# Optimization experiments

Hardware: AMD Instinct MI355X
Metric: run time of the kernel (lower is better)

## Reference

```python
import jax, jax.numpy as jnp
import numpy as np

K = 3
STRIDE = 1
PAD = 1


def conv2d(x, w, b):
    # standard NCHW conv, stride 1, pad 1
    out = jax.lax.conv_general_dilated(
        x, w, (STRIDE, STRIDE), [(PAD, PAD), (PAD, PAD)],
        dimension_numbers=("NCHW", "OIHW", "NCHW"))
    return out + b[None, :, None, None]


def deform_conv2d(x, offset, mask, weight):
    # torchvision.ops.deform_conv2d semantics (offset_groups=1):
    # offset: [B, 2*K*K, Ho, Wo] laid out as (k, (y, x)) per kernel tap k (row-major)
    # mask:   [B, K*K, Ho, Wo]
    B, C, H, W = x.shape
    KK = K * K
    Ho, Wo = offset.shape[2:]
    off = offset.reshape(B, KK, 2, Ho, Wo)

    # base sampling positions: p = out*stride - pad + kernel_tap + offset
    tap_y = jnp.repeat(jnp.arange(K, dtype=x.dtype), K)  # [KK]
    tap_x = jnp.tile(jnp.arange(K, dtype=x.dtype), K)    # [KK]
    grid_y = jnp.arange(Ho, dtype=x.dtype) * STRIDE - PAD
    grid_x = jnp.arange(Wo, dtype=x.dtype) * STRIDE - PAD
    py = grid_y[None, None, :, None] + tap_y[None, :, None, None] + off[:, :, 0]  # [B,KK,Ho,Wo]
    px = grid_x[None, None, None, :] + tap_x[None, :, None, None] + off[:, :, 1]

    y0 = jnp.floor(py)
    x0 = jnp.floor(px)
    wy1 = py - y0  # fractional parts
    wx1 = px - x0

    xf = x.reshape(B, C, H * W)

    def gather(yi, xi):
        # zero-padding semantics: out-of-bounds corners contribute 0
        valid = (yi >= 0) & (yi <= H - 1) & (xi >= 0) & (xi <= W - 1)
        idx = (jnp.clip(yi, 0, H - 1) * W + jnp.clip(xi, 0, W - 1)).astype(jnp.int32)
        v = jnp.take_along_axis(xf, idx.reshape(B, 1, KK * Ho * Wo), axis=2)
        v = v.reshape(B, C, KK, Ho, Wo)
        return v * valid[:, None].astype(x.dtype)

    e = lambda a: a[:, None]  # [B,KK,Ho,Wo] -> [B,1,KK,Ho,Wo]
    sampled = (gather(y0, x0) * e((1 - wy1) * (1 - wx1))
               + gather(y0, x0 + 1) * e((1 - wy1) * wx1)
               + gather(y0 + 1, x0) * e(wy1 * (1 - wx1))
               + gather(y0 + 1, x0 + 1) * e(wy1 * wx1))
    sampled = sampled * mask[:, None]  # modulated, [B,C,KK,Ho,Wo]

    Cout = weight.shape[0]
    out = jnp.einsum("bckhw,ock->bohw", sampled, weight.reshape(Cout, C, KK))
    return out


def setup_inputs() -> dict:
    key = jax.random.key(0)
    ks = jax.random.split(key, 5)
    B, Cin, Cout, H, W = 4, 128, 256, 64, 64
    x = jax.random.normal(ks[0], (B, Cin, H, W), jnp.float32)
    # offset/modulator convs are zero-init in the module; use small random weights
    # so the deformable sampling path is actually exercised
    offset_w = jax.random.normal(ks[1], (2 * K * K, Cin, K, K), jnp.float32) * 0.02
    offset_b = jax.random.normal(ks[2], (2 * K * K,), jnp.float32) * 0.1
    mod_w = jax.random.normal(ks[3], (K * K, Cin, K, K), jnp.float32) * 0.02
    mod_b = jnp.zeros((K * K,), jnp.float32)
    weight = jax.random.normal(ks[4], (Cout, Cin, K, K), jnp.float32) * (1.0 / np.sqrt(Cin * K * K))
    return {"x": x, "offset_w": offset_w, "offset_b": offset_b,
            "mod_w": mod_w, "mod_b": mod_b, "weight": weight}


def reference(x, offset_w, offset_b, mod_w, mod_b, weight):
    H, W = x.shape[2], x.shape[3]
    max_offset = max(H, W) / 4.0
    offset = jnp.clip(conv2d(x, offset_w, offset_b), -max_offset, max_offset)
    mask = 2.0 * jax.nn.sigmoid(conv2d(x, mod_w, mod_b))
    return deform_conv2d(x, offset, mask, weight)
```

## Files before the change

### kernel.cpp

```cpp
#include <hip/hip_runtime.h>
#include <math.h>

#define CIN   128
#define COUT  256
#define HH    64
#define WW    64
#define BB    4
#define KK    9
#define CK    (CIN*KK)

typedef unsigned short u16;
typedef unsigned int   u32;
using f32x4  = __attribute__((ext_vector_type(4))) float;
using s16x8  = __attribute__((ext_vector_type(8))) short;

__device__ __forceinline__ u16 f2bf(float f) {
    union { float f; u32 u; } v; v.f = f;
    u32 u = v.u;
    u += 0x7FFFu + ((u >> 16) & 1u);
    return (u16)(u >> 16);
}
__device__ __forceinline__ float bfel(s16x8 v, int j) {
    union { u32 u; float f; } c; c.u = ((u32)(u16)v[j]) << 16; return c.f;
}
__device__ __forceinline__ u32 asu(float f) {
    union { float f; u32 u; } v; v.f = f; return v.u;
}

__global__ __launch_bounds__(256)
void prep_all(const float* __restrict__ x, const float* __restrict__ w,
              const float* __restrict__ ow, const float* __restrict__ mw,
              u16* __restrict__ xt, u16* __restrict__ wfrag,
              u16* __restrict__ wofsf) {
    __shared__ u16 T[64][130];
    int blk = blockIdx.x;
    int tid = threadIdx.x;

    if (blk < 256) {
        int b = blk >> 6, y = blk & 63;
        int lane = tid & 63, cw = tid >> 6;
        for (int c = cw; c < 128; c += 4)
            T[lane][c] = f2bf(x[((b * 128 + c) * 64 + y) * 64 + lane]);
        __syncthreads();
        int c = tid & 127;
        for (int p = tid >> 7; p < 64; p += 2)
            xt[((b * 64 + y) * 64 + p) * 128 + c] = T[p][c];
    } else if (blk < 256 + 1152) {
        int i = (blk - 256) * 256 + tid;
        int j    = i & 7;
        int lane = (i >> 3) & 63;
        int ks4  = (i >> 9) & 3;
        int t    = (i >> 11) & 1;
        int wv   = (i >> 12) & 7;
        int tap  = i >> 15;
        int co = (wv * 2 + t) * 16 + (lane & 15);
        int k  = tap * 128 + ks4 * 32 + (lane >> 4) * 8 + j;
        int c  = k & 127;
        wfrag[i] = f2bf(w[co * CK + c * 9 + tap]);
    } else {
        int i = (blk - 1408) * 256 + tid;
        if (i < 9 * 4096) {
            int j    = i & 7;
            int lane = (i >> 3) & 63;
            int ks4  = (i >> 9) & 3;
            int t    = (i >> 11) & 1;
            int tap  = i >> 12;
            int co = t * 16 + (lane & 15);
            int k  = tap * 128 + ks4 * 32 + (lane >> 4) * 8 + j;
            int c  = k & 127;
            float v = 0.f;
            if (co < 18)      v = ow[co * CK + c * 9 + tap];
            else if (co < 27) v = mw[(co - 18) * CK + c * 9 + tap];
            wofsf[i] = f2bf(v);
        }
    }
}

__global__ __launch_bounds__(512, 4)
void dcn_fused(const u16* __restrict__ xt, const u16* __restrict__ wofsf,
               const float* __restrict__ ob, const float* __restrict__ mb,
               const u16* __restrict__ wfrag, float* __restrict__ out) {
    int blkid = blockIdx.x;
    int xcd = blkid & 7, idx = blkid >> 3;
    int b   = xcd >> 1;
    int ho  = ((xcd & 1) << 5) + (idx >> 1);
    int wo0 = (idx & 1) << 5;
    int tid = threadIdx.x;

    __shared__ __align__(16) u16 Sm[2][32][136];
    __shared__ float s_om[27][32];
    __shared__ int   s_idx[32][KK][4];
    __shared__ float s_wgt[32][KK][4];

    int wv   = tid >> 6, lane = tid & 63;
    int quad = lane >> 4, l16 = lane & 15;
    int gpx  = wv * 4 + (lane >> 4);
    int oct  = lane & 15;

    const u16* xtb = xt + (size_t)b * 4096 * 128;
    const s16x8 vzero = {0,0,0,0,0,0,0,0};

    int pa_ph = wv & 1;
    f32x4 aco[2];
    aco[0] = (f32x4)(0.f); aco[1] = (f32x4)(0.f);

    s16x8 sreg[2];
    auto pa_gather = [&](int tap, int slot) {
        int kx = tap % 3;
        int y  = ho - 1 + tap / 3;
        bool yok = (unsigned)y < HH;
        int col = wo0 + gpx + kx - 1;
        bool ok = yok && ((unsigned)col < WW);
        int yc = yok ? y : 0;
        int cc = ((unsigned)col < WW) ? col : 0;
        s16x8 v = *(const s16x8*)(xtb + (size_t)(yc * 64 + cc) * 128 + oct * 8);
        sreg[slot] = ok ? v : vzero;
    };

    pa_gather(0, 0);
    pa_gather(1, 1);
    int buf = 0;
#pragma unroll
    for (int tap = 0; tap < 9; ++tap) {
        int sl = tap & 1;
        *(s16x8*)(&Sm[buf][gpx][oct * 8]) = sreg[sl];
        __syncthreads();
        if (tap + 2 < 9) pa_gather(tap + 2, sl);

        if (wv < 2) {
            const u16* wc = wofsf + tap * 4096 + lane * 8;
#pragma unroll
            for (int ks4 = 0; ks4 < 4; ++ks4) {
                s16x8 bfrag = *(const s16x8*)(&Sm[buf][pa_ph * 16 + l16][ks4 * 32 + quad * 8]);
#pragma unroll
                for (int t = 0; t < 2; ++t) {
                    s16x8 afrag = *(const s16x8*)(wc + (t * 4 + ks4) * 512);
                    aco[t] = __builtin_amdgcn_mfma_f32_16x16x32_bf16(afrag, bfrag, aco[t], 0, 0, 0);
                }
            }
        }
        buf ^= 1;
    }
    if (wv < 2) {
#pragma unroll
        for (int t = 0; t < 2; ++t) {
#pragma unroll
            for (int r = 0; r < 4; ++r) {
                int co = t * 16 + quad * 4 + r;
                if (co < 27) {
                    float v = aco[t][r];
                    if (co < 18) {
                        v += ob[co];
                        v = fminf(fmaxf(v, -16.f), 16.f);
                    } else {
                        v += mb[co - 18];
                        v = 2.f / (1.f + expf(-v));
                    }
                    s_om[co][pa_ph * 16 + l16] = v;
                }
            }
        }
    }
    __syncthreads();

    if (tid < 32 * KK) {
        int p = tid / KK, k = tid - (tid / KK) * KK;
        int wo = wo0 + p;
        float offy = s_om[2 * k][p];
        float offx = s_om[2 * k + 1][p];
        float mval = s_om[18 + k][p];

        float py = (float)(ho - 1 + k / 3) + offy;
        float px = (float)(wo - 1 + k % 3) + offx;
        float y0f = floorf(py), x0f = floorf(px);
        float wy1 = py - y0f,  wx1 = px - x0f;
        float wy0 = 1.f - wy1, wx0 = 1.f - wx1;
        int iy0 = (int)y0f, ix0 = (int)x0f;
        int iy1 = iy0 + 1,  ix1 = ix0 + 1;
        bool vy0 = (iy0 >= 0) && (iy0 < HH);
        bool vy1 = (iy1 >= 0) && (iy1 < HH);
        bool vx0 = (ix0 >= 0) && (ix0 < WW);
        bool vx1 = (ix1 >= 0) && (ix1 < WW);
        int cy0 = min(max(iy0, 0), HH - 1), cy1 = min(max(iy1, 0), HH - 1);
        int cx0 = min(max(ix0, 0), WW - 1), cx1 = min(max(ix1, 0), WW - 1);
        s_idx[p][k][0] = (cy0 * WW + cx0) * 128;
        s_idx[p][k][1] = (cy0 * WW + cx1) * 128;
        s_idx[p][k][2] = (cy1 * WW + cx0) * 128;
        s_idx[p][k][3] = (cy1 * WW + cx1) * 128;
        s_wgt[p][k][0] = (vy0 && vx0) ? mval * wy0 * wx0 : 0.f;
        s_wgt[p][k][1] = (vy0 && vx1) ? mval * wy0 * wx1 : 0.f;
        s_wgt[p][k][2] = (vy1 && vx0) ? mval * wy1 * wx0 : 0.f;
        s_wgt[p][k][3] = (vy1 && vx1) ? mval * wy1 * wx1 : 0.f;
    }
    __syncthreads();

    f32x4 acc[2][2];
#pragma unroll
    for (int t = 0; t < 2; ++t) { acc[t][0] = (f32x4)(0.f); acc[t][1] = (f32x4)(0.f); }

    s16x8 crs[2][4];
    float gs[2][4];
    auto gatherB = [&](int tap, int slot) {
        int i0 = s_idx[gpx][tap][0], i1 = s_idx[gpx][tap][1];
        int i2 = s_idx[gpx][tap][2], i3 = s_idx[gpx][tap][3];
        gs[slot][0] = s_wgt[gpx][tap][0]; gs[slot][1] = s_wgt[gpx][tap][1];
        gs[slot][2] = s_wgt[gpx][tap][2]; gs[slot][3] = s_wgt[gpx][tap][3];
        int co8 = oct * 8;
        crs[slot][0] = *(const s16x8*)(xtb + i0 + co8);
        crs[slot][1] = *(const s16x8*)(xtb + i1 + co8);
        crs[slot][2] = *(const s16x8*)(xtb + i2 + co8);
        crs[slot][3] = *(const s16x8*)(xtb + i3 + co8);
    };

    gatherB(0, 0);
    gatherB(1, 1);
    buf = 0;
#pragma unroll
    for (int tap = 0; tap < 9; ++tap) {
        int sl = tap & 1;
        float g0 = gs[sl][0], g1 = gs[sl][1], g2 = gs[sl][2], g3 = gs[sl][3];
        float o[8];
#pragma unroll
        for (int j = 0; j < 8; ++j)
            o[j] = g0 * bfel(crs[sl][0], j) + g1 * bfel(crs[sl][1], j)
                 + g2 * bfel(crs[sl][2], j) + g3 * bfel(crs[sl][3], j);
        uint4 pkv;
        pkv.x = (asu(o[1]) & 0xFFFF0000u) | (asu(o[0]) >> 16);
        pkv.y = (asu(o[3]) & 0xFFFF0000u) | (asu(o[2]) >> 16);
        pkv.z = (asu(o[5]) & 0xFFFF0000u) | (asu(o[4]) >> 16);
        pkv.w = (asu(o[7]) & 0xFFFF0000u) | (asu(o[6]) >> 16);
        *(uint4*)(&Sm[buf][gpx][oct * 8]) = pkv;
        __syncthreads();

        if (tap + 2 < 9) gatherB(tap + 2, sl);

        const u16* wc = wfrag + (tap * 8 + wv) * 4096 + lane * 8;
        s16x8 af[8];
#pragma unroll
        for (int t = 0; t < 2; ++t)
#pragma unroll
            for (int ks4 = 0; ks4 < 4; ++ks4)
                af[t * 4 + ks4] = *(const s16x8*)(wc + (t * 4 + ks4) * 512);

#pragma unroll
        for (int ks4 = 0; ks4 < 4; ++ks4) {
            s16x8 bf0 = *(const s16x8*)(&Sm[buf][l16][ks4 * 32 + quad * 8]);
            s16x8 bf1 = *(const s16x8*)(&Sm[buf][16 + l16][ks4 * 32 + quad * 8]);
#pragma unroll
            for (int t = 0; t < 2; ++t) {
                acc[t][0] = __builtin_amdgcn_mfma_f32_16x16x32_bf16(af[t * 4 + ks4], bf0, acc[t][0], 0, 0, 0);
                acc[t][1] = __builtin_amdgcn_mfma_f32_16x16x32_bf16(af[t * 4 + ks4], bf1, acc[t][1], 0, 0, 0);
            }
        }
        buf ^= 1;
    }

#pragma unroll
    for (int t = 0; t < 2; ++t) {
        int cobase = (wv * 2 + t) * 16 + quad * 4;
#pragma unroll
        for (int ph = 0; ph < 2; ++ph) {
#pragma unroll
            for (int r = 0; r < 4; ++r) {
                int co = cobase + r;
                out[((b * COUT + co) * HH + ho) * WW + wo0 + ph * 16 + l16] = acc[t][ph][r];
            }
        }
    }
}

extern "C" void kernel_launch(void* const* d_in, const int* in_sizes, int n_in,
                              void* d_out, int out_size, void* d_ws, size_t ws_size,
                              hipStream_t stream) {
    const float* x  = (const float*)d_in[0];
    const float* ow = (const float*)d_in[1];
    const float* ob = (const float*)d_in[2];
    const float* mw = (const float*)d_in[3];
    const float* mb = (const float*)d_in[4];
    const float* wt = (const float*)d_in[5];

    char* ws = (char*)d_ws;
    u16* wfrag = (u16*)ws;  ws += (size_t)COUT * CK * 2;
    u16* wofsf = (u16*)ws;  ws += (size_t)32 * CK * 2;
    u16* xt    = (u16*)ws;
    float* out = (float*)d_out;

    prep_all<<<1552, 256, 0, stream>>>(x, wt, ow, mw, xt, wfrag, wofsf);

    dcn_fused<<<BB * HH * 2, 512, 0, stream>>>(xt, wofsf, ob, mb, wfrag, out);
}
```

Before: 103.6 us.

## Process two taps per barrier with four-slot LDS ring in both phases

Both the offset/mask conv phase and the deformable gather-GEMM phase now handle taps in pairs. Each pair writes two LDS slots, then takes one barrier, then prefetches the next pair. This cuts __syncthreads from 9 to 5 per phase and doubles the loads in flight. The cost is a larger LDS buffer (4 slots), more live registers for the doubled prefetch state, and possibly lower occupancy.

Result: no change. 103.6 us, median of 2 (-0.0%).

```diff
diff --git a/kernel.cpp b/kernel.cpp
--- a/kernel.cpp
+++ b/kernel.cpp
@@ -87,7 +87,7 @@
     int wo0 = (idx & 1) << 5;
     int tid = threadIdx.x;
 
-    __shared__ __align__(16) u16 Sm[2][32][136];
+    __shared__ __align__(16) u16 Sm[4][32][136];
     __shared__ float s_om[27][32];
     __shared__ int   s_idx[32][KK][4];
     __shared__ float s_wgt[32][KK][4];
@@ -104,8 +104,8 @@
     f32x4 aco[2];
     aco[0] = (f32x4)(0.f); aco[1] = (f32x4)(0.f);
 
-    s16x8 sreg[2];
-    auto pa_gather = [&](int tap, int slot) {
+    s16x8 sA[2][2];
+    auto pa_gather = [&](int tap, int sp, int ti) {
         int kx = tap % 3;
         int y  = ho - 1 + tap / 3;
         bool yok = (unsigned)y < HH;
@@ -114,33 +114,41 @@
         int yc = yok ? y : 0;
         int cc = ((unsigned)col < WW) ? col : 0;
         s16x8 v = *(const s16x8*)(xtb + (size_t)(yc * 64 + cc) * 128 + oct * 8);
-        sreg[slot] = ok ? v : vzero;
-    };
-
-    pa_gather(0, 0);
-    pa_gather(1, 1);
-    int buf = 0;
-#pragma unroll
-    for (int tap = 0; tap < 9; ++tap) {
-        int sl = tap & 1;
-        *(s16x8*)(&Sm[buf][gpx][oct * 8]) = sreg[sl];
+        sA[sp][ti] = ok ? v : vzero;
+    };
+
+    auto pa_mfma_tap = [&](int tap, int slot) {
+        const u16* wc = wofsf + tap * 4096 + lane * 8;
+#pragma unroll
+        for (int ks4 = 0; ks4 < 4; ++ks4) {
+            s16x8 bfrag = *(const s16x8*)(&Sm[slot][pa_ph * 16 + l16][ks4 * 32 + quad * 8]);
+#pragma unroll
+            for (int t = 0; t < 2; ++t) {
+                s16x8 afrag = *(const s16x8*)(wc + (t * 4 + ks4) * 512);
+                aco[t] = __builtin_amdgcn_mfma_f32_16x16x32_bf16(afrag, bfrag, aco[t], 0, 0, 0);
+            }
+        }
+    };
+
+    pa_gather(0, 0, 0);
+    pa_gather(1, 0, 1);
+#pragma unroll
+    for (int p = 0; p < 4; ++p) {
+        int sp = p & 1;
+        *(s16x8*)(&Sm[2 * sp    ][gpx][oct * 8]) = sA[sp][0];
+        *(s16x8*)(&Sm[2 * sp + 1][gpx][oct * 8]) = sA[sp][1];
         __syncthreads();
-        if (tap + 2 < 9) pa_gather(tap + 2, sl);
-
+        if (p < 3) { pa_gather(2 * p + 2, sp ^ 1, 0); pa_gather(2 * p + 3, sp ^ 1, 1); }
+        else       { pa_gather(8,         sp ^ 1, 0); }
         if (wv < 2) {
-            const u16* wc = wofsf + tap * 4096 + lane * 8;
-#pragma unroll
-            for (int ks4 = 0; ks4 < 4; ++ks4) {
-                s16x8 bfrag = *(const s16x8*)(&Sm[buf][pa_ph * 16 + l16][ks4 * 32 + quad * 8]);
-#pragma unroll
-                for (int t = 0; t < 2; ++t) {
-                    s16x8 afrag = *(const s16x8*)(wc + (t * 4 + ks4) * 512);
-                    aco[t] = __builtin_amdgcn_mfma_f32_16x16x32_bf16(afrag, bfrag, aco[t], 0, 0, 0);
-                }
-            }
-        }
-        buf ^= 1;
-    }
+            pa_mfma_tap(2 * p,     2 * sp);
+            pa_mfma_tap(2 * p + 1, 2 * sp + 1);
+        }
+    }
+    *(s16x8*)(&Sm[0][gpx][oct * 8]) = sA[0][0];
+    __syncthreads();
+    if (wv < 2) pa_mfma_tap(8, 0);
+
     if (wv < 2) {
 #pragma unroll
         for (int t = 0; t < 2; ++t) {
@@ -198,42 +206,37 @@
 #pragma unroll
     for (int t = 0; t < 2; ++t) { acc[t][0] = (f32x4)(0.f); acc[t][1] = (f32x4)(0.f); }
 
-    s16x8 crs[2][4];
-    float gs[2][4];
-    auto gatherB = [&](int tap, int slot) {
+    s16x8 crs[2][2][4];
+    float gs[2][2][4];
+    auto gatherB = [&](int tap, int sp, int ti) {
         int i0 = s_idx[gpx][tap][0], i1 = s_idx[gpx][tap][1];
         int i2 = s_idx[gpx][tap][2], i3 = s_idx[gpx][tap][3];
-        gs[slot][0] = s_wgt[gpx][tap][0]; gs[slot][1] = s_wgt[gpx][tap][1];
-        gs[slot][2] = s_wgt[gpx][tap][2]; gs[slot][3] = s_wgt[gpx][tap][3];
+        gs[sp][ti][0] = s_wgt[gpx][tap][0]; gs[sp][ti][1] = s_wgt[gpx][tap][1];
+        gs[sp][ti][2] = s_wgt[gpx][tap][2]; gs[sp][ti][3] = s_wgt[gpx][tap][3];
         int co8 = oct * 8;
-        crs[slot][0] = *(const s16x8*)(xtb + i0 + co8);
-        crs[slot][1] = *(const s16x8*)(xtb + i1 + co8);
-        crs[slot][2] = *(const s16x8*)(xtb + i2 + co8);
-        crs[slot][3] = *(const s16x8*)(xtb + i3 + co8);
-    };
-
-    gatherB(0, 0);
-    gatherB(1, 1);
-    buf = 0;
-#pragma unroll
-    for (int tap = 0; tap < 9; ++tap) {
-        int sl = tap & 1;
-        float g0 = gs[sl][0], g1 = gs[sl][1], g2 = gs[sl][2], g3 = gs[sl][3];
+        crs[sp][ti][0] = *(const s16x8*)(xtb + i0 + co8);
+        crs[sp][ti][1] = *(const s16x8*)(xtb + i1 + co8);
+        crs[sp][ti][2] = *(const s16x8*)(xtb + i2 + co8);
+        crs[sp][ti][3] = *(const s16x8*)(xtb + i3 + co8);
+    };
+
+    auto blend_store = [&](int sp, int ti, int slot) {
+        float g0 = gs[sp][ti][0], g1 = gs[sp][ti][1];
+        float g2 = gs[sp][ti][2], g3 = gs[sp][ti][3];
         float o[8];
 #pragma unroll
         for (int j = 0; j < 8; ++j)
-            o[j] = g0 * bfel(crs[sl][0], j) + g1 * bfel(crs[sl][1], j)
-                 + g2 * bfel(crs[sl][2], j) + g3 * bfel(crs[sl][3], j);
+            o[j] = g0 * bfel(crs[sp][ti][0], j) + g1 * bfel(crs[sp][ti][1], j)
+                 + g2 * bfel(crs[sp][ti][2], j) + g3 * bfel(crs[sp][ti][3], j);
         uint4 pkv;
         pkv.x = (asu(o[1]) & 0xFFFF0000u) | (asu(o[0]) >> 16);
         pkv.y = (asu(o[3]) & 0xFFFF0000u) | (asu(o[2]) >> 16);
         pkv.z = (asu(o[5]) & 0xFFFF0000u) | (asu(o[4]) >> 16);
         pkv.w = (asu(o[7]) & 0xFFFF0000u) | (asu(o[6]) >> 16);
-        *(uint4*)(&Sm[buf][gpx][oct * 8]) = pkv;
-        __syncthreads();
-
-        if (tap + 2 < 9) gatherB(tap + 2, sl);
-
+        *(uint4*)(&Sm[slot][gpx][oct * 8]) = pkv;
+    };
+
+    auto pb_mfma_tap = [&](int tap, int slot) {
         const u16* wc = wfrag + (tap * 8 + wv) * 4096 + lane * 8;
         s16x8 af[8];
 #pragma unroll
@@ -241,19 +244,34 @@
 #pragma unroll
             for (int ks4 = 0; ks4 < 4; ++ks4)
                 af[t * 4 + ks4] = *(const s16x8*)(wc + (t * 4 + ks4) * 512);
-
 #pragma unroll
         for (int ks4 = 0; ks4 < 4; ++ks4) {
-            s16x8 bf0 = *(const s16x8*)(&Sm[buf][l16][ks4 * 32 + quad * 8]);
-            s16x8 bf1 = *(const s16x8*)(&Sm[buf][16 + l16][ks4 * 32 + quad * 8]);
+            s16x8 bf0 = *(const s16x8*)(&Sm[slot][l16][ks4 * 32 + quad * 8]);
+            s16x8 bf1 = *(const s16x8*)(&Sm[slot][16 + l16][ks4 * 32 + quad * 8]);
 #pragma unroll
             for (int t = 0; t < 2; ++t) {
                 acc[t][0] = __builtin_amdgcn_mfma_f32_16x16x32_bf16(af[t * 4 + ks4], bf0, acc[t][0], 0, 0, 0);
                 acc[t][1] = __builtin_amdgcn_mfma_f32_16x16x32_bf16(af[t * 4 + ks4], bf1, acc[t][1], 0, 0, 0);
             }
         }
-        buf ^= 1;
-    }
+    };
+
+    gatherB(0, 0, 0);
+    gatherB(1, 0, 1);
+#pragma unroll
+    for (int p = 0; p < 4; ++p) {
+        int sp = p & 1;
+        blend_store(sp, 0, 2 * sp);
+        blend_store(sp, 1, 2 * sp + 1);
+        __syncthreads();
+        if (p < 3) { gatherB(2 * p + 2, sp ^ 1, 0); gatherB(2 * p + 3, sp ^ 1, 1); }
+        else       { gatherB(8,         sp ^ 1, 0); }
+        pb_mfma_tap(2 * p,     2 * sp);
+        pb_mfma_tap(2 * p + 1, 2 * sp + 1);
+    }
+    blend_store(0, 0, 0);
+    __syncthreads();
+    pb_mfma_tap(8, 0);
 
 #pragma unroll
     for (int t = 0; t < 2; ++t) {
```
